# Optimization experiments

Hardware: AMD Instinct MI355X
Metric: run time of the kernel (lower is better)

## Reference

```python
import jax, jax.numpy as jnp
import numpy as np

TAU = 75.0            # smoothing temperature (km)
EARTH_RADIUS = 6371.0 # km
B = 4096              # batch size
C = 12288             # num geocell classes
EPS = 1e-9


def pairwise_haversine(latlon, centroids):
    """latlon: [B,2] degrees, centroids: [C,2] degrees -> [B,C] km."""
    ll = jnp.radians(latlon)
    cc = jnp.radians(centroids)
    lat1, lon1 = ll[:, 0:1], ll[:, 1:2]   # [B,1]
    lat2, lon2 = cc[None, :, 0], cc[None, :, 1]  # [1,C]
    dlat = lat2 - lat1
    dlon = lon2 - lon1
    a = jnp.sin(dlat / 2) ** 2 + jnp.cos(lat1) * jnp.cos(lat2) * jnp.sin(dlon / 2) ** 2
    c = 2.0 * jnp.arcsin(jnp.sqrt(a))
    return EARTH_RADIUS * c  # [B,C]


def setup_inputs() -> dict:
    key = jax.random.key(0)
    k1, k2, k3, k4, k5, k6 = jax.random.split(key, 6)
    pred_logits = jax.random.normal(k1, (B, C), dtype=jnp.float32)
    latlon = jnp.stack([
        jax.random.uniform(k2, (B,), minval=-90.0, maxval=90.0),
        jax.random.uniform(k3, (B,), minval=-180.0, maxval=180.0),
    ], axis=1).astype(jnp.float32)
    centroids = jnp.stack([
        jax.random.uniform(k4, (C,), minval=-90.0, maxval=90.0),
        jax.random.uniform(k5, (C,), minval=-180.0, maxval=180.0),
    ], axis=1).astype(jnp.float32)
    geocell_indices = jax.random.randint(k6, (B,), 0, C, dtype=jnp.int64)
    return {"pred_logits": pred_logits, "latlon": latlon,
            "centroids": centroids, "geocell_indices": geocell_indices}


def reference(pred_logits, latlon, centroids, geocell_indices):
    # Haversine-smoothed target distribution per sample
    dist = pairwise_haversine(latlon, centroids)        # [B,C]
    w = jnp.exp(-dist / TAU)                            # [B,C]
    target_probs = w / jnp.sum(w, axis=1, keepdims=True)
    # Original computes log(softmax(x) + 1e-9), not log_softmax
    pred_probs = jax.nn.softmax(pred_logits, axis=1)
    loss = jnp.mean(jnp.sum(-target_probs * jnp.log(pred_probs + EPS), axis=1))
    return loss
```

## Files before the change

### kernel.cpp

```cpp
#include <hip/hip_runtime.h>
#include <math.h>

namespace {
constexpr int B_ = 4096;
constexpr int C_ = 12288;
constexpr int R_ = 2;
constexpr float DEG2RAD = 0.017453292519943295f;
constexpr float LOG2E = 1.4426950408889634f;
constexpr float KN2 = -245.10427f;
constexpr float C0 = KN2;
constexpr float C1 = KN2 / 6.0f;
constexpr float C2 = KN2 * 0.075f;
constexpr float C3 = KN2 * 0.0446428571f;
}

__global__ void centroid_xyz_kernel(const float* __restrict__ centroids,
                                    float* __restrict__ ctq) {
    int c = blockIdx.x * blockDim.x + threadIdx.x;
    if (c >= C_) return;
    float lat = centroids[2 * c] * DEG2RAD;
    float lon = centroids[2 * c + 1] * DEG2RAD;
    float cl = cosf(lat);
    int g = c >> 2, j = c & 3;
    ctq[12 * g + j]     = 0.5f * cl * cosf(lon);
    ctq[12 * g + 4 + j] = 0.5f * cl * sinf(lon);
    ctq[12 * g + 8 + j] = 0.5f * sinf(lat);
}

__device__ __forceinline__ float wave_red_add(float v) {
#pragma unroll
    for (int off = 32; off > 0; off >>= 1) v += __shfl_down(v, off, 64);
    return v;
}

__device__ __forceinline__ void accum_pair(float lv, float xv, float yv, float zv,
                                           float x1, float y1, float z1,
                                           float& W, float& T, float& S) {
    float dx = xv - x1, dy = yv - y1, dz = zv - z1;
    float a = fmaf(dx, dx, fmaf(dy, dy, dz * dz));
    float s = __builtin_amdgcn_sqrtf(a);
    float p = fmaf(a, C3, C2);
    p = fmaf(a, p, C1);
    p = fmaf(a, p, C0);
    float w = __builtin_amdgcn_exp2f(s * p);
    W += w;
    T = fmaf(w, lv, T);
    S += __builtin_amdgcn_exp2f(lv * LOG2E);
}

__global__ __launch_bounds__(256) void row_loss_kernel(
    const float* __restrict__ logits, const float* __restrict__ latlon,
    const float* __restrict__ ctq, float* __restrict__ row_loss) {
    const int b0 = blockIdx.x * R_;

    float x1[R_], y1[R_], z1[R_];
#pragma unroll
    for (int r = 0; r < R_; ++r) {
        float lat = latlon[2 * (b0 + r)] * DEG2RAD;
        float lon = latlon[2 * (b0 + r) + 1] * DEG2RAD;
        float cl = cosf(lat);
        x1[r] = 0.5f * cl * cosf(lon);
        y1[r] = 0.5f * cl * sinf(lon);
        z1[r] = 0.5f * sinf(lat);
    }

    const float4* __restrict__ ct4 = (const float4*)ctq + 3 * (size_t)threadIdx.x;
    const float4* __restrict__ L0 =
        (const float4*)(logits + (size_t)b0 * C_) + threadIdx.x;
    const float4* __restrict__ L1 =
        (const float4*)(logits + (size_t)(b0 + 1) * C_) + threadIdx.x;

    float W[R_], T[R_], S[R_];
#pragma unroll
    for (int r = 0; r < R_; ++r) { W[r] = 0.f; T[r] = 0.f; S[r] = 0.f; }

#pragma unroll 2
    for (int i = 0; i < C_ / 4 / 256; ++i) {
        float4 X = ct4[0];
        float4 Y = ct4[1];
        float4 Z = ct4[2];
        float4 la = *L0;
        float4 lb = *L1;
        accum_pair(la.x, X.x, Y.x, Z.x, x1[0], y1[0], z1[0], W[0], T[0], S[0]);
        accum_pair(la.y, X.y, Y.y, Z.y, x1[0], y1[0], z1[0], W[0], T[0], S[0]);
        accum_pair(la.z, X.z, Y.z, Z.z, x1[0], y1[0], z1[0], W[0], T[0], S[0]);
        accum_pair(la.w, X.w, Y.w, Z.w, x1[0], y1[0], z1[0], W[0], T[0], S[0]);
        accum_pair(lb.x, X.x, Y.x, Z.x, x1[1], y1[1], z1[1], W[1], T[1], S[1]);
        accum_pair(lb.y, X.y, Y.y, Z.y, x1[1], y1[1], z1[1], W[1], T[1], S[1]);
        accum_pair(lb.z, X.z, Y.z, Z.z, x1[1], y1[1], z1[1], W[1], T[1], S[1]);
        accum_pair(lb.w, X.w, Y.w, Z.w, x1[1], y1[1], z1[1], W[1], T[1], S[1]);
        ct4 += 3 * 256;
        L0 += 256;
        L1 += 256;
    }

    __shared__ float red[3][R_][4];
    const int lane = threadIdx.x & 63, wv = threadIdx.x >> 6;
#pragma unroll
    for (int r = 0; r < R_; ++r) {
        float Wr = wave_red_add(W[r]);
        float Tr = wave_red_add(T[r]);
        float Sr = wave_red_add(S[r]);
        if (lane == 0) { red[0][r][wv] = Wr; red[1][r][wv] = Tr; red[2][r][wv] = Sr; }
    }
    __syncthreads();
    if (threadIdx.x < R_) {
        int r = threadIdx.x;
        float Wt = red[0][r][0] + red[0][r][1] + red[0][r][2] + red[0][r][3];
        float Tt = red[1][r][0] + red[1][r][1] + red[1][r][2] + red[1][r][3];
        float St = red[2][r][0] + red[2][r][1] + red[2][r][2] + red[2][r][3];
        Wt = fmaxf(Wt, 1e-30f);
        row_loss[b0 + r] = logf(St) - Tt / Wt;
    }
}

__global__ __launch_bounds__(256) void final_reduce_kernel(
    const float* __restrict__ row_loss, float* __restrict__ out) {
    float s = 0.f;
    for (int i = threadIdx.x; i < B_; i += 256) s += row_loss[i];
    s = wave_red_add(s);
    __shared__ float red[4];
    const int lane = threadIdx.x & 63, wv = threadIdx.x >> 6;
    if (lane == 0) red[wv] = s;
    __syncthreads();
    if (threadIdx.x == 0)
        out[0] = (red[0] + red[1] + red[2] + red[3]) * (1.0f / B_);
}

extern "C" void kernel_launch(void* const* d_in, const int* in_sizes, int n_in,
                              void* d_out, int out_size, void* d_ws, size_t ws_size,
                              hipStream_t stream) {
    const float* pred_logits = (const float*)d_in[0];
    const float* latlon      = (const float*)d_in[1];
    const float* centroids   = (const float*)d_in[2];
    float* ctq      = (float*)d_ws;
    float* row_loss = ctq + 3 * C_;
    float* out      = (float*)d_out;

    centroid_xyz_kernel<<<(C_ + 255) / 256, 256, 0, stream>>>(centroids, ctq);
    row_loss_kernel<<<B_ / R_, 256, 0, stream>>>(pred_logits, latlon, ctq, row_loss);
    final_reduce_kernel<<<1, 256, 0, stream>>>(row_loss, out);
}
```

Baseline: 47.69 us.

## Drop final reduce kernel via atomics, truncate distance polynomial, raise occupancy hint

Removes the separate final reduction launch: the first kernel zeroes the output and each block atomically adds its row losses, scaled by 1/B, directly into it. The arcsin-based distance polynomial is cut from four terms to two, which saves FMAs per element but makes the smoothing weights less accurate at larger distances. It also adds a min-blocks-per-CU launch bound of 8 to push higher occupancy. Risks include float atomic contention and nondeterministic summation order, and the coarser approximation could break the correctness tolerance.

```diff
diff --git a/kernel.cpp b/kernel.cpp
--- a/kernel.cpp
+++ b/kernel.cpp
@@ -10,13 +10,13 @@
 constexpr float KN2 = -245.10427f;
 constexpr float C0 = KN2;
 constexpr float C1 = KN2 / 6.0f;
-constexpr float C2 = KN2 * 0.075f;
-constexpr float C3 = KN2 * 0.0446428571f;
 }
 
 __global__ void centroid_xyz_kernel(const float* __restrict__ centroids,
-                                    float* __restrict__ ctq) {
+                                    float* __restrict__ ctq,
+                                    float* __restrict__ out) {
     int c = blockIdx.x * blockDim.x + threadIdx.x;
+    if (c == 0) out[0] = 0.0f;
     if (c >= C_) return;
     float lat = centroids[2 * c] * DEG2RAD;
     float lon = centroids[2 * c + 1] * DEG2RAD;
@@ -39,18 +39,16 @@
     float dx = xv - x1, dy = yv - y1, dz = zv - z1;
     float a = fmaf(dx, dx, fmaf(dy, dy, dz * dz));
     float s = __builtin_amdgcn_sqrtf(a);
-    float p = fmaf(a, C3, C2);
-    p = fmaf(a, p, C1);
-    p = fmaf(a, p, C0);
+    float p = fmaf(a, C1, C0);
     float w = __builtin_amdgcn_exp2f(s * p);
     W += w;
     T = fmaf(w, lv, T);
     S += __builtin_amdgcn_exp2f(lv * LOG2E);
 }
 
-__global__ __launch_bounds__(256) void row_loss_kernel(
+__global__ __launch_bounds__(256, 8) void row_loss_kernel(
     const float* __restrict__ logits, const float* __restrict__ latlon,
-    const float* __restrict__ ctq, float* __restrict__ row_loss) {
+    const float* __restrict__ ctq, float* __restrict__ out) {
     const int b0 = blockIdx.x * R_;
 
     float x1[R_], y1[R_], z1[R_];
@@ -110,21 +108,9 @@
         float Tt = red[1][r][0] + red[1][r][1] + red[1][r][2] + red[1][r][3];
         float St = red[2][r][0] + red[2][r][1] + red[2][r][2] + red[2][r][3];
         Wt = fmaxf(Wt, 1e-30f);
-        row_loss[b0 + r] = logf(St) - Tt / Wt;
+        float loss = logf(St) - Tt / Wt;
+        atomicAdd(out, loss * (1.0f / B_));
     }
-}
-
-__global__ __launch_bounds__(256) void final_reduce_kernel(
-    const float* __restrict__ row_loss, float* __restrict__ out) {
-    float s = 0.f;
-    for (int i = threadIdx.x; i < B_; i += 256) s += row_loss[i];
-    s = wave_red_add(s);
-    __shared__ float red[4];
-    const int lane = threadIdx.x & 63, wv = threadIdx.x >> 6;
-    if (lane == 0) red[wv] = s;
-    __syncthreads();
-    if (threadIdx.x == 0)
-        out[0] = (red[0] + red[1] + red[2] + red[3]) * (1.0f / B_);
 }
 
 extern "C" void kernel_launch(void* const* d_in, const int* in_sizes, int n_in,
@@ -133,11 +119,9 @@
     const float* pred_logits = (const float*)d_in[0];
     const float* latlon      = (const float*)d_in[1];
     const float* centroids   = (const float*)d_in[2];
-    float* ctq      = (float*)d_ws;
-    float* row_loss = ctq + 3 * C_;
-    float* out      = (float*)d_out;
+    float* ctq = (float*)d_ws;
+    float* out = (float*)d_out;
 
-    centroid_xyz_kernel<<<(C_ + 255) / 256, 256, 0, stream>>>(centroids, ctq);
-    row_loss_kernel<<<B_ / R_, 256, 0, stream>>>(pred_logits, latlon, ctq, row_loss);
-    final_reduce_kernel<<<1, 256, 0, stream>>>(row_loss, out);
+    centroid_xyz_kernel<<<(C_ + 255) / 256, 256, 0, stream>>>(centroids, ctq, out);
+    row_loss_kernel<<<B_ / R_, 256, 0, stream>>>(pred_logits, latlon, ctq, out);
 }
```

After: 57.46 us. 20.5% more time.
